# Kernel optimization log

Hardware: AMD Instinct MI355X
Metric: run time of the kernel (lower is better)

## Reference

```python
import jax, jax.numpy as jnp
import numpy as np

D_K = 128


def setup_inputs() -> dict:
    key = jax.random.key(0)
    kq, kk, kv = jax.random.split(key, 3)
    S = 8192
    Query = jax.random.normal(kq, (S, D_K), dtype=jnp.float32)
    Key = jax.random.normal(kk, (S, D_K), dtype=jnp.float32)
    Value = jax.random.normal(kv, (S, D_K), dtype=jnp.float32)
    return {"Query": Query, "Key": Key, "Value": Value}


def reference(Query, Key, Value):
    # scaled dot-product attention, unmasked (masked=False default)
    scale = 1.0 / jnp.sqrt(jnp.asarray(D_K, dtype=jnp.float32))
    scores = jnp.matmul(Query, Key.T) * scale          # [S, S]
    attn = jax.nn.softmax(scores, axis=1)              # softmax over keys (dim=1 on 2-D)
    delta_E = jnp.matmul(attn, Value)                  # [S, d_k]
    return delta_E
```

## Files before the change

### kernel.cpp

```cpp
#include <hip/hip_runtime.h>

#define S_LEN 8192
#define D_KK  128
#define SCALE 0.08838834764831845f

typedef __bf16 bf16x2 __attribute__((ext_vector_type(2)));
typedef __bf16 bf16x4 __attribute__((ext_vector_type(4)));
typedef __bf16 bf16x8 __attribute__((ext_vector_type(8)));
typedef float  f32x16 __attribute__((ext_vector_type(16)));

__global__ __launch_bounds__(256) void prep_kv_23450521436217(
    const float* __restrict__ K,
    const float* __restrict__ V,
    __bf16* __restrict__ Kf,
    __bf16* __restrict__ Vf)
{
    const int tid = threadIdx.x;
    const int t   = blockIdx.x;
    __shared__ __bf16 T[32][140];

    const float* ktile = K + (size_t)t * 32 * D_KK;
    const float* vtile = V + (size_t)t * 32 * D_KK;

    const int row = tid & 31;
    const int cp  = tid >> 5;
    #pragma unroll
    for (int i = 0; i < 2; ++i) {
        int c = cp * 2 + i;
        int s = c >> 1, hi = c & 1;
        const float* src = ktile + row * D_KK + c * 8;
        float4 a = *(const float4*)(src);
        float4 b = *(const float4*)(src + 4);
        bf16x8 o;
        o[0]=(__bf16)a.x; o[1]=(__bf16)a.y; o[2]=(__bf16)a.z; o[3]=(__bf16)a.w;
        o[4]=(__bf16)b.x; o[5]=(__bf16)b.y; o[6]=(__bf16)b.z; o[7]=(__bf16)b.w;
        *(bf16x8*)(Kf + (size_t)(t * 8 + s) * 512 + hi * 256 + row * 8) = o;
    }

    #pragma unroll
    for (int i = 0; i < 4; ++i) {
        int f4 = tid + i * 256;
        float4 v = ((const float4*)vtile)[f4];
        int r = f4 >> 5, cc = (f4 & 31) << 2;
        bf16x4 b;
        b[0]=(__bf16)v.x; b[1]=(__bf16)v.y; b[2]=(__bf16)v.z; b[3]=(__bf16)v.w;
        *(bf16x4*)(&T[r][cc]) = b;
    }
    __syncthreads();

    #pragma unroll
    for (int i = 0; i < 2; ++i) {
        int idx  = tid + i * 256;
        int frag = idx >> 6, lane = idx & 63;
        int hi = lane >> 5, l5 = lane & 31;
        int d = frag >> 1, h = frag & 1;
        bf16x8 o;
        #pragma unroll
        for (int j = 0; j < 8; ++j) o[j] = T[16 * h + 8 * hi + j][32 * d + l5];
        *(bf16x8*)(Vf + (size_t)(t * 8 + frag) * 512 + lane * 8) = o;
    }
}

__global__ __launch_bounds__(512, 2) void attn_fwd_23450521436217(
    const float*  __restrict__ Q,
    const __bf16* __restrict__ Kf,
    const __bf16* __restrict__ Vf,
    float* __restrict__ O)
{
    const int tid  = threadIdx.x;
    const int wave = tid >> 6;
    const int lane = tid & 63;
    const int l5   = lane & 31;
    const int hi   = lane >> 5;

    __shared__ float Oacc[D_KK][33];
    __shared__ float Ml[8][32], Ll[8][32], Lf[32];

    const int qrow = blockIdx.x * 32 + l5;

    bf16x8 qf[8];
    #pragma unroll
    for (int s = 0; s < 8; ++s) {
        const float* qp = Q + (size_t)qrow * D_KK + s * 16 + hi * 8;
        float4 a = *(const float4*)(qp);
        float4 b = *(const float4*)(qp + 4);
        bf16x8 f;
        f[0]=(__bf16)(a.x*SCALE); f[1]=(__bf16)(a.y*SCALE);
        f[2]=(__bf16)(a.z*SCALE); f[3]=(__bf16)(a.w*SCALE);
        f[4]=(__bf16)(b.x*SCALE); f[5]=(__bf16)(b.y*SCALE);
        f[6]=(__bf16)(b.z*SCALE); f[7]=(__bf16)(b.w*SCALE);
        qf[s] = f;
    }

    f32x16 oacc[4];
    #pragma unroll
    for (int d = 0; d < 4; ++d) oacc[d] = f32x16{};
    float m_run = -1e30f, l_run = 0.0f;

    const __bf16* kfp = Kf + (size_t)(wave * 32) * 4096 + lane * 8;
    const __bf16* vfp = Vf + (size_t)(wave * 32) * 4096 + lane * 8;

    bf16x8 kbufA[8], kbufB[8], vb[8];

    #pragma unroll
    for (int s = 0; s < 8; ++s) kbufA[s] = *(const bf16x8*)(kfp + s * 512);

#define ATTN_BODY(KC, KN, IT, PF)                                              \
    {                                                                          \
        const __bf16* vt = vfp + (size_t)(IT) * 4096;                          \
        _Pragma("unroll")                                                      \
        for (int f = 0; f < 8; ++f)                                            \
            vb[f] = *(const bf16x8*)(vt + f * 512);                            \
                 \
        f32x16 c = f32x16{};                                                   \
        _Pragma("unroll")                                                      \
        for (int s = 0; s < 8; ++s)                                            \
            c = __builtin_amdgcn_mfma_f32_32x32x16_bf16(KC[s], qf[s], c,       \
                                                        0, 0, 0);             \
                                  \
        if (PF) {                                                              \
            const __bf16* kn = kfp + (size_t)((IT) + 1) * 4096;                \
            _Pragma("unroll")                                                  \
            for (int s = 0; s < 8; ++s)                                        \
                KN[s] = *(const bf16x8*)(kn + s * 512);                        \
        }                                                                      \
                  \
        float tmax = c[0];                                                     \
        _Pragma("unroll")                                                      \
        for (int r = 1; r < 16; ++r) tmax = fmaxf(tmax, c[r]);                 \
        tmax = fmaxf(tmax, __shfl_xor(tmax, 32));                              \
        if (__any(tmax > m_run + 8.0f)) {                                      \
            float mnew  = fmaxf(m_run, tmax);                                  \
            float alpha = __expf(m_run - mnew);                                \
            _Pragma("unroll")                                                  \
            for (int d = 0; d < 4; ++d) oacc[d] *= alpha;                      \
            l_run *= alpha;                                                    \
            m_run  = mnew;                                                     \
        }                                                                      \
        float p[16], ps = 0.0f;                                                \
        _Pragma("unroll")                                                      \
        for (int r = 0; r < 16; ++r) { p[r] = __expf(c[r] - m_run); ps += p[r]; } \
        ps += __shfl_xor(ps, 32);                                              \
        l_run += ps;                                                           \
                   \
        unsigned pk[8];                                                        \
        _Pragma("unroll")                                                      \
        for (int tq = 0; tq < 8; ++tq) {                                       \
            bf16x2 w; w[0] = (__bf16)p[2*tq]; w[1] = (__bf16)p[2*tq+1];        \
            pk[tq] = __builtin_bit_cast(unsigned, w);                          \
        }                                                                      \
        asm volatile("v_permlane32_swap_b32 %0, %1" : "+v"(pk[0]), "+v"(pk[2]));\
        asm volatile("v_permlane32_swap_b32 %0, %1" : "+v"(pk[1]), "+v"(pk[3]));\
        asm volatile("v_permlane32_swap_b32 %0, %1" : "+v"(pk[4]), "+v"(pk[6]));\
        asm volatile("v_permlane32_swap_b32 %0, %1" : "+v"(pk[5]), "+v"(pk[7]));\
        union { unsigned u[4]; bf16x8 f; } b0, b1;                             \
        b0.u[0]=pk[0]; b0.u[1]=pk[1]; b0.u[2]=pk[2]; b0.u[3]=pk[3];            \
        b1.u[0]=pk[4]; b1.u[1]=pk[5]; b1.u[2]=pk[6]; b1.u[3]=pk[7];            \
                                               \
        _Pragma("unroll")                                                      \
        for (int d = 0; d < 4; ++d) {                                          \
            oacc[d] = __builtin_amdgcn_mfma_f32_32x32x16_bf16(vb[2*d+0], b0.f, \
                                                              oacc[d], 0,0,0); \
            oacc[d] = __builtin_amdgcn_mfma_f32_32x32x16_bf16(vb[2*d+1], b1.f, \
                                                              oacc[d], 0,0,0); \
        }                                                                      \
    }

    for (int it = 0; it < 32; it += 2) {
        ATTN_BODY(kbufA, kbufB, it,     1);
        ATTN_BODY(kbufB, kbufA, it + 1, (it + 2 < 32));
    }
#undef ATTN_BODY

    if (lane < 32) { Ml[wave][lane] = m_run; Ll[wave][lane] = l_run; }
    __syncthreads();

    float M = Ml[0][l5];
    #pragma unroll
    for (int w = 1; w < 8; ++w) M = fmaxf(M, Ml[w][l5]);
    float L = 0.0f;
    #pragma unroll
    for (int w = 0; w < 8; ++w) L += Ll[w][l5] * __expf(Ml[w][l5] - M);
    if (tid < 32) Lf[tid] = L;

    const float wscale = __expf(m_run - M);

    for (int r = 0; r < 8; ++r) {
        if (wave == r) {
            #pragma unroll
            for (int d = 0; d < 4; ++d)
                #pragma unroll
                for (int reg = 0; reg < 16; ++reg) {
                    int drow = d * 32 + (reg & 3) + 8 * (reg >> 2) + 4 * hi;
                    float v = oacc[d][reg] * wscale;
                    if (r == 0) Oacc[drow][l5]  = v;
                    else        Oacc[drow][l5] += v;
                }
        }
        __syncthreads();
    }

    const int q  = tid >> 4;
    const int d0 = (tid & 15) * 8;
    const float invl = 1.0f / Lf[q];
    float4 o1, o2;
    o1.x = Oacc[d0+0][q] * invl; o1.y = Oacc[d0+1][q] * invl;
    o1.z = Oacc[d0+2][q] * invl; o1.w = Oacc[d0+3][q] * invl;
    o2.x = Oacc[d0+4][q] * invl; o2.y = Oacc[d0+5][q] * invl;
    o2.z = Oacc[d0+6][q] * invl; o2.w = Oacc[d0+7][q] * invl;
    float* op = O + (size_t)(blockIdx.x * 32 + q) * D_KK + d0;
    *(float4*)(op)     = o1;
    *(float4*)(op + 4) = o2;
}

extern "C" void kernel_launch(void* const* d_in, const int* in_sizes, int n_in,
                              void* d_out, int out_size, void* d_ws, size_t ws_size,
                              hipStream_t stream) {
    const float* Q = (const float*)d_in[0];
    const float* K = (const float*)d_in[1];
    const float* V = (const float*)d_in[2];
    float* O = (float*)d_out;

    __bf16* Kf = (__bf16*)d_ws;
    __bf16* Vf = (__bf16*)((char*)d_ws + (size_t)S_LEN*D_KK*2);

    hipLaunchKernelGGL(prep_kv_23450521436217, dim3(S_LEN/32), dim3(256), 0, stream,
                       K, V, Kf, Vf);
    hipLaunchKernelGGL(attn_fwd_23450521436217, dim3(S_LEN/32), dim3(512), 0, stream,
                       Q, Kf, Vf, O);
}
```

Baseline: 65.15 us.

## Software-pipeline QK^T one tile ahead of softmax and PV in attention loop

Restructures the main attention loop so the QK^T MFMA for the next key tile is issued before the softmax and PV work of the current tile. Key loads are prefetched two tiles ahead through double-buffered score accumulators. MFMA sections are wrapped in s_setprio to raise wave priority, and the max and sum reductions become tree-shaped to shorten dependency chains. The aim is to overlap matrix-core work with the exp and shuffle latency, at the cost of more VGPRs for the second score accumulator and the extra key buffer.

```diff
diff --git a/kernel.cpp b/kernel.cpp
--- a/kernel.cpp
+++ b/kernel.cpp
@@ -100,34 +100,52 @@
     const __bf16* kfp = Kf + (size_t)(wave * 32) * 4096 + lane * 8;
     const __bf16* vfp = Vf + (size_t)(wave * 32) * 4096 + lane * 8;
 
-    bf16x8 kbufA[8], kbufB[8], vb[8];
-
-    #pragma unroll
-    for (int s = 0; s < 8; ++s) kbufA[s] = *(const bf16x8*)(kfp + s * 512);
-
-#define ATTN_BODY(KC, KN, IT, PF)                                              \
+    bf16x8 kA[8], kB[8], vb[8];
+    f32x16 c0, c1;
+
+    #pragma unroll
+    for (int s = 0; s < 8; ++s) kA[s] = *(const bf16x8*)(kfp + s * 512);
+    #pragma unroll
+    for (int s = 0; s < 8; ++s) kB[s] = *(const bf16x8*)(kfp + 4096 + s * 512);
+    c0 = f32x16{};
+    __builtin_amdgcn_s_setprio(1);
+    #pragma unroll
+    for (int s = 0; s < 8; ++s)
+        c0 = __builtin_amdgcn_mfma_f32_32x32x16_bf16(kA[s], qf[s], c0, 0, 0, 0);
+    __builtin_amdgcn_s_setprio(0);
+
+#define ATTN_BODY(CCUR, CNEXT, KNEXT, KPF, IT, DO_QK, DO_PF)                   \
     {                                                                          \
+          \
         const __bf16* vt = vfp + (size_t)(IT) * 4096;                          \
         _Pragma("unroll")                                                      \
         for (int f = 0; f < 8; ++f)                                            \
             vb[f] = *(const bf16x8*)(vt + f * 512);                            \
-                 \
-        f32x16 c = f32x16{};                                                   \
-        _Pragma("unroll")                                                      \
-        for (int s = 0; s < 8; ++s)                                            \
-            c = __builtin_amdgcn_mfma_f32_32x32x16_bf16(KC[s], qf[s], c,       \
-                                                        0, 0, 0);             \
-                                  \
-        if (PF) {                                                              \
-            const __bf16* kn = kfp + (size_t)((IT) + 1) * 4096;                \
+                \
+        if (DO_QK) {                                                           \
+            CNEXT = f32x16{};                                                  \
+            __builtin_amdgcn_s_setprio(1);                                     \
             _Pragma("unroll")                                                  \
             for (int s = 0; s < 8; ++s)                                        \
-                KN[s] = *(const bf16x8*)(kn + s * 512);                        \
+                CNEXT = __builtin_amdgcn_mfma_f32_32x32x16_bf16(KNEXT[s],      \
+                                                        qf[s], CNEXT, 0,0,0); \
+            __builtin_amdgcn_s_setprio(0);                                     \
         }                                                                      \
                   \
-        float tmax = c[0];                                                     \
-        _Pragma("unroll")                                                      \
-        for (int r = 1; r < 16; ++r) tmax = fmaxf(tmax, c[r]);                 \
+        if (DO_PF) {                                                           \
+            const __bf16* kn = kfp + (size_t)((IT) + 2) * 4096;                \
+            _Pragma("unroll")                                                  \
+            for (int s = 0; s < 8; ++s)                                        \
+                KPF[s] = *(const bf16x8*)(kn + s * 512);                       \
+        }                                                                      \
+                     \
+        float x0 = fmaxf(CCUR[0], CCUR[8]),  x1 = fmaxf(CCUR[1], CCUR[9]);     \
+        float x2 = fmaxf(CCUR[2], CCUR[10]), x3 = fmaxf(CCUR[3], CCUR[11]);    \
+        float x4 = fmaxf(CCUR[4], CCUR[12]), x5 = fmaxf(CCUR[5], CCUR[13]);    \
+        float x6 = fmaxf(CCUR[6], CCUR[14]), x7 = fmaxf(CCUR[7], CCUR[15]);    \
+        float y0 = fmaxf(fmaxf(x0, x4), fmaxf(x1, x5));                        \
+        float y1 = fmaxf(fmaxf(x2, x6), fmaxf(x3, x7));                        \
+        float tmax = fmaxf(y0, y1);                                            \
         tmax = fmaxf(tmax, __shfl_xor(tmax, 32));                              \
         if (__any(tmax > m_run + 8.0f)) {                                      \
             float mnew  = fmaxf(m_run, tmax);                                  \
@@ -137,9 +155,12 @@
             l_run *= alpha;                                                    \
             m_run  = mnew;                                                     \
         }                                                                      \
-        float p[16], ps = 0.0f;                                                \
-        _Pragma("unroll")                                                      \
-        for (int r = 0; r < 16; ++r) { p[r] = __expf(c[r] - m_run); ps += p[r]; } \
+        float p[16];                                                           \
+        _Pragma("unroll")                                                      \
+        for (int r = 0; r < 16; ++r) p[r] = __expf(CCUR[r] - m_run);           \
+        float s0a = (p[0]+p[1]) + (p[2]+p[3]),  s1a = (p[4]+p[5]) + (p[6]+p[7]); \
+        float s2a = (p[8]+p[9]) + (p[10]+p[11]), s3a = (p[12]+p[13]) + (p[14]+p[15]); \
+        float ps = (s0a + s1a) + (s2a + s3a);                                  \
         ps += __shfl_xor(ps, 32);                                              \
         l_run += ps;                                                           \
                    \
@@ -156,7 +177,8 @@
         union { unsigned u[4]; bf16x8 f; } b0, b1;                             \
         b0.u[0]=pk[0]; b0.u[1]=pk[1]; b0.u[2]=pk[2]; b0.u[3]=pk[3];            \
         b1.u[0]=pk[4]; b1.u[1]=pk[5]; b1.u[2]=pk[6]; b1.u[3]=pk[7];            \
-                                               \
+                                                 \
+        __builtin_amdgcn_s_setprio(1);                                         \
         _Pragma("unroll")                                                      \
         for (int d = 0; d < 4; ++d) {                                          \
             oacc[d] = __builtin_amdgcn_mfma_f32_32x32x16_bf16(vb[2*d+0], b0.f, \
@@ -164,12 +186,15 @@
             oacc[d] = __builtin_amdgcn_mfma_f32_32x32x16_bf16(vb[2*d+1], b1.f, \
                                                               oacc[d], 0,0,0); \
         }                                                                      \
-    }
-
-    for (int it = 0; it < 32; it += 2) {
-        ATTN_BODY(kbufA, kbufB, it,     1);
-        ATTN_BODY(kbufB, kbufA, it + 1, (it + 2 < 32));
-    }
+        __builtin_amdgcn_s_setprio(0);                                         \
+    }
+
+    for (int it = 0; it < 30; it += 2) {
+        ATTN_BODY(c0, c1, kB, kA, it,     1, 1);
+        ATTN_BODY(c1, c0, kA, kB, it + 1, 1, 1);
+    }
+    ATTN_BODY(c0, c1, kB, kA, 30, 1, 0);
+    ATTN_BODY(c1, c0, kA, kB, 31, 0, 0);
 #undef ATTN_BODY
 
     if (lane < 32) { Ml[wave][lane] = m_run; Ll[wave][lane] = l_run; }
```

New measurement: 64.75 us. No clear change (-0.6%).

## Share K tiles across waves via LDS and split-K with separate merge kernel

Applied to the files above, without the earlier changes.

Restructures the attention kernel so each block owns 8 query sub-tiles (one per wave) and a 1/8 slice of the keys. K tiles are staged into LDS with global_load_lds double buffering and shared by all waves, instead of each wave streaming its own K from global memory. Partial outputs are written as fp16 along with per-slice max and sum, and a new merge kernel combines them. This cuts K global traffic and removes the in-block cross-wave reduction, but adds a third launch, partial-output memory traffic, fp16 rounding of the partials, and a per-iteration block barrier.

```diff
diff --git a/kernel.cpp b/kernel.cpp
--- a/kernel.cpp
+++ b/kernel.cpp
@@ -8,6 +8,7 @@
 typedef __bf16 bf16x4 __attribute__((ext_vector_type(4)));
 typedef __bf16 bf16x8 __attribute__((ext_vector_type(8)));
 typedef float  f32x16 __attribute__((ext_vector_type(16)));
+typedef _Float16 half_t;
 
 __global__ __launch_bounds__(256) void prep_kv_23450521436217(
     const float* __restrict__ K,
@@ -61,11 +62,13 @@
     }
 }
 
-__global__ __launch_bounds__(512, 2) void attn_fwd_23450521436217(
+__global__ __launch_bounds__(512, 2) void attn_part_23450521436217(
     const float*  __restrict__ Q,
     const __bf16* __restrict__ Kf,
     const __bf16* __restrict__ Vf,
-    float* __restrict__ O)
+    half_t* __restrict__ P16,
+    float*  __restrict__ Mp,
+    float*  __restrict__ Lp)
 {
     const int tid  = threadIdx.x;
     const int wave = tid >> 6;
@@ -73,10 +76,12 @@
     const int l5   = lane & 31;
     const int hi   = lane >> 5;
 
-    __shared__ float Oacc[D_KK][33];
-    __shared__ float Ml[8][32], Ll[8][32], Lf[32];
-
-    const int qrow = blockIdx.x * 32 + l5;
+    const int ks   = blockIdx.x & 7;
+    const int qt   = blockIdx.x >> 3;
+    const int qsub = qt * 8 + wave;
+    const int qrow = qsub * 32 + l5;
+
+    __shared__ __align__(16) __bf16 Klds[2][4096];
 
     bf16x8 qf[8];
     #pragma unroll
@@ -97,120 +102,171 @@
     for (int d = 0; d < 4; ++d) oacc[d] = f32x16{};
     float m_run = -1e30f, l_run = 0.0f;
 
-    const __bf16* kfp = Kf + (size_t)(wave * 32) * 4096 + lane * 8;
-    const __bf16* vfp = Vf + (size_t)(wave * 32) * 4096 + lane * 8;
-
-    bf16x8 kbufA[8], kbufB[8], vb[8];
-
-    #pragma unroll
-    for (int s = 0; s < 8; ++s) kbufA[s] = *(const bf16x8*)(kfp + s * 512);
-
-#define ATTN_BODY(KC, KN, IT, PF)                                              \
-    {                                                                          \
-        const __bf16* vt = vfp + (size_t)(IT) * 4096;                          \
-        _Pragma("unroll")                                                      \
-        for (int f = 0; f < 8; ++f)                                            \
-            vb[f] = *(const bf16x8*)(vt + f * 512);                            \
-                 \
-        f32x16 c = f32x16{};                                                   \
-        _Pragma("unroll")                                                      \
-        for (int s = 0; s < 8; ++s)                                            \
-            c = __builtin_amdgcn_mfma_f32_32x32x16_bf16(KC[s], qf[s], c,       \
-                                                        0, 0, 0);             \
-                                  \
-        if (PF) {                                                              \
-            const __bf16* kn = kfp + (size_t)((IT) + 1) * 4096;                \
-            _Pragma("unroll")                                                  \
-            for (int s = 0; s < 8; ++s)                                        \
-                KN[s] = *(const bf16x8*)(kn + s * 512);                        \
-        }                                                                      \
-                  \
-        float tmax = c[0];                                                     \
-        _Pragma("unroll")                                                      \
-        for (int r = 1; r < 16; ++r) tmax = fmaxf(tmax, c[r]);                 \
-        tmax = fmaxf(tmax, __shfl_xor(tmax, 32));                              \
-        if (__any(tmax > m_run + 8.0f)) {                                      \
-            float mnew  = fmaxf(m_run, tmax);                                  \
-            float alpha = __expf(m_run - mnew);                                \
-            _Pragma("unroll")                                                  \
-            for (int d = 0; d < 4; ++d) oacc[d] *= alpha;                      \
-            l_run *= alpha;                                                    \
-            m_run  = mnew;                                                     \
-        }                                                                      \
-        float p[16], ps = 0.0f;                                                \
-        _Pragma("unroll")                                                      \
-        for (int r = 0; r < 16; ++r) { p[r] = __expf(c[r] - m_run); ps += p[r]; } \
-        ps += __shfl_xor(ps, 32);                                              \
-        l_run += ps;                                                           \
-                   \
-        unsigned pk[8];                                                        \
-        _Pragma("unroll")                                                      \
-        for (int tq = 0; tq < 8; ++tq) {                                       \
-            bf16x2 w; w[0] = (__bf16)p[2*tq]; w[1] = (__bf16)p[2*tq+1];        \
-            pk[tq] = __builtin_bit_cast(unsigned, w);                          \
-        }                                                                      \
-        asm volatile("v_permlane32_swap_b32 %0, %1" : "+v"(pk[0]), "+v"(pk[2]));\
-        asm volatile("v_permlane32_swap_b32 %0, %1" : "+v"(pk[1]), "+v"(pk[3]));\
-        asm volatile("v_permlane32_swap_b32 %0, %1" : "+v"(pk[4]), "+v"(pk[6]));\
-        asm volatile("v_permlane32_swap_b32 %0, %1" : "+v"(pk[5]), "+v"(pk[7]));\
-        union { unsigned u[4]; bf16x8 f; } b0, b1;                             \
-        b0.u[0]=pk[0]; b0.u[1]=pk[1]; b0.u[2]=pk[2]; b0.u[3]=pk[3];            \
-        b1.u[0]=pk[4]; b1.u[1]=pk[5]; b1.u[2]=pk[6]; b1.u[3]=pk[7];            \
-                                               \
-        _Pragma("unroll")                                                      \
-        for (int d = 0; d < 4; ++d) {                                          \
-            oacc[d] = __builtin_amdgcn_mfma_f32_32x32x16_bf16(vb[2*d+0], b0.f, \
-                                                              oacc[d], 0,0,0); \
-            oacc[d] = __builtin_amdgcn_mfma_f32_32x32x16_bf16(vb[2*d+1], b1.f, \
-                                                              oacc[d], 0,0,0); \
-        }                                                                      \
-    }
-
-    for (int it = 0; it < 32; it += 2) {
-        ATTN_BODY(kbufA, kbufB, it,     1);
-        ATTN_BODY(kbufB, kbufA, it + 1, (it + 2 < 32));
-    }
-#undef ATTN_BODY
-
-    if (lane < 32) { Ml[wave][lane] = m_run; Ll[wave][lane] = l_run; }
-    __syncthreads();
-
-    float M = Ml[0][l5];
-    #pragma unroll
-    for (int w = 1; w < 8; ++w) M = fmaxf(M, Ml[w][l5]);
-    float L = 0.0f;
-    #pragma unroll
-    for (int w = 0; w < 8; ++w) L += Ll[w][l5] * __expf(Ml[w][l5] - M);
-    if (tid < 32) Lf[tid] = L;
-
-    const float wscale = __expf(m_run - M);
-
-    for (int r = 0; r < 8; ++r) {
-        if (wave == r) {
+    const __bf16* kbase = Kf + (size_t)(ks * 32) * 4096;
+    const __bf16* vfp   = Vf + (size_t)(ks * 32) * 4096 + lane * 8;
+
+    {
+        const __bf16* src = kbase + wave * 512 + lane * 8;
+        __builtin_amdgcn_global_load_lds(
+            (const __attribute__((address_space(1))) void*)src,
+            (__attribute__((address_space(3))) void*)&Klds[0][wave * 512],
+            16, 0, 0);
+    }
+    __syncthreads();
+
+    for (int it = 0; it < 32; ++it) {
+        const int cur = it & 1;
+
+        if (it < 31) {
+            const __bf16* src = kbase + (size_t)(it + 1) * 4096 + wave * 512 + lane * 8;
+            __builtin_amdgcn_global_load_lds(
+                (const __attribute__((address_space(1))) void*)src,
+                (__attribute__((address_space(3))) void*)&Klds[cur ^ 1][wave * 512],
+                16, 0, 0);
+        }
+
+        const __bf16* vt = vfp + (size_t)it * 4096;
+        bf16x8 vb[8];
+        #pragma unroll
+        for (int f = 0; f < 8; ++f) vb[f] = *(const bf16x8*)(vt + f * 512);
+
+        f32x16 c = f32x16{};
+        __builtin_amdgcn_s_setprio(1);
+        #pragma unroll
+        for (int s = 0; s < 8; ++s) {
+            bf16x8 kf = *(const bf16x8*)(&Klds[cur][s * 512 + lane * 8]);
+            c = __builtin_amdgcn_mfma_f32_32x32x16_bf16(kf, qf[s], c, 0, 0, 0);
+        }
+        __builtin_amdgcn_s_setprio(0);
+
+        float x0 = fmaxf(c[0], c[8]),  x1 = fmaxf(c[1], c[9]);
+        float x2 = fmaxf(c[2], c[10]), x3 = fmaxf(c[3], c[11]);
+        float x4 = fmaxf(c[4], c[12]), x5 = fmaxf(c[5], c[13]);
+        float x6 = fmaxf(c[6], c[14]), x7 = fmaxf(c[7], c[15]);
+        float y0 = fmaxf(fmaxf(x0, x4), fmaxf(x1, x5));
+        float y1 = fmaxf(fmaxf(x2, x6), fmaxf(x3, x7));
+        float tmax = fmaxf(y0, y1);
+        tmax = fmaxf(tmax, __shfl_xor(tmax, 32));
+        if (__any(tmax > m_run + 8.0f)) {
+            float mnew  = fmaxf(m_run, tmax);
+            float alpha = __expf(m_run - mnew);
             #pragma unroll
-            for (int d = 0; d < 4; ++d)
-                #pragma unroll
-                for (int reg = 0; reg < 16; ++reg) {
-                    int drow = d * 32 + (reg & 3) + 8 * (reg >> 2) + 4 * hi;
-                    float v = oacc[d][reg] * wscale;
-                    if (r == 0) Oacc[drow][l5]  = v;
-                    else        Oacc[drow][l5] += v;
-                }
-        }
+            for (int d = 0; d < 4; ++d) oacc[d] *= alpha;
+            l_run *= alpha;
+            m_run  = mnew;
+        }
+        float p[16];
+        #pragma unroll
+        for (int r = 0; r < 16; ++r) p[r] = __expf(c[r] - m_run);
+        float s0a = (p[0]+p[1]) + (p[2]+p[3]),   s1a = (p[4]+p[5]) + (p[6]+p[7]);
+        float s2a = (p[8]+p[9]) + (p[10]+p[11]), s3a = (p[12]+p[13]) + (p[14]+p[15]);
+        float ps = (s0a + s1a) + (s2a + s3a);
+        ps += __shfl_xor(ps, 32);
+        l_run += ps;
+
+        unsigned pk[8];
+        #pragma unroll
+        for (int tq = 0; tq < 8; ++tq) {
+            bf16x2 w; w[0] = (__bf16)p[2*tq]; w[1] = (__bf16)p[2*tq+1];
+            pk[tq] = __builtin_bit_cast(unsigned, w);
+        }
+        asm volatile("v_permlane32_swap_b32 %0, %1" : "+v"(pk[0]), "+v"(pk[2]));
+        asm volatile("v_permlane32_swap_b32 %0, %1" : "+v"(pk[1]), "+v"(pk[3]));
+        asm volatile("v_permlane32_swap_b32 %0, %1" : "+v"(pk[4]), "+v"(pk[6]));
+        asm volatile("v_permlane32_swap_b32 %0, %1" : "+v"(pk[5]), "+v"(pk[7]));
+        union { unsigned u[4]; bf16x8 f; } b0, b1;
+        b0.u[0]=pk[0]; b0.u[1]=pk[1]; b0.u[2]=pk[2]; b0.u[3]=pk[3];
+        b1.u[0]=pk[4]; b1.u[1]=pk[5]; b1.u[2]=pk[6]; b1.u[3]=pk[7];
+
+        __builtin_amdgcn_s_setprio(1);
+        #pragma unroll
+        for (int d = 0; d < 4; ++d) {
+            oacc[d] = __builtin_amdgcn_mfma_f32_32x32x16_bf16(vb[2*d+0], b0.f,
+                                                              oacc[d], 0,0,0);
+            oacc[d] = __builtin_amdgcn_mfma_f32_32x32x16_bf16(vb[2*d+1], b1.f,
+                                                              oacc[d], 0,0,0);
+        }
+        __builtin_amdgcn_s_setprio(0);
+
         __syncthreads();
     }
 
-    const int q  = tid >> 4;
-    const int d0 = (tid & 15) * 8;
-    const float invl = 1.0f / Lf[q];
-    float4 o1, o2;
-    o1.x = Oacc[d0+0][q] * invl; o1.y = Oacc[d0+1][q] * invl;
-    o1.z = Oacc[d0+2][q] * invl; o1.w = Oacc[d0+3][q] * invl;
-    o2.x = Oacc[d0+4][q] * invl; o2.y = Oacc[d0+5][q] * invl;
-    o2.z = Oacc[d0+6][q] * invl; o2.w = Oacc[d0+7][q] * invl;
-    float* op = O + (size_t)(blockIdx.x * 32 + q) * D_KK + d0;
-    *(float4*)(op)     = o1;
-    *(float4*)(op + 4) = o2;
+    if (lane < 32) {
+        Mp[ks * S_LEN + qrow] = m_run;
+        Lp[ks * S_LEN + qrow] = l_run;
+    }
+    half_t* pb = P16 + (size_t)(ks * 256 + qsub) * (128 * 32);
+    #pragma unroll
+    for (int d = 0; d < 4; ++d)
+        #pragma unroll
+        for (int reg = 0; reg < 16; ++reg) {
+            int drow = d * 32 + (reg & 3) + 8 * (reg >> 2) + 4 * hi;
+            pb[drow * 32 + l5] = (half_t)oacc[d][reg];
+        }
+}
+
+__global__ __launch_bounds__(256) void attn_merge_23450521436217(
+    const half_t* __restrict__ P16,
+    const float*  __restrict__ Mp,
+    const float*  __restrict__ Lp,
+    float* __restrict__ O)
+{
+    const int tid  = threadIdx.x;
+    const int qsub = blockIdx.x;
+
+    __shared__ float W[8][32];
+    __shared__ float Li[32];
+    __shared__ float Ot[128][33];
+
+    if (tid < 32) {
+        const int qrow = qsub * 32 + tid;
+        float m[8], l[8];
+        #pragma unroll
+        for (int ks = 0; ks < 8; ++ks) {
+            m[ks] = Mp[ks * S_LEN + qrow];
+            l[ks] = Lp[ks * S_LEN + qrow];
+        }
+        float M = m[0];
+        #pragma unroll
+        for (int ks = 1; ks < 8; ++ks) M = fmaxf(M, m[ks]);
+        float L = 0.0f;
+        #pragma unroll
+        for (int ks = 0; ks < 8; ++ks) {
+            float w = __expf(m[ks] - M);
+            W[ks][tid] = w;
+            L += l[ks] * w;
+        }
+        Li[tid] = 1.0f / L;
+    }
+    __syncthreads();
+
+    const int q  = tid & 31;
+    const int dg = tid >> 5;
+    #pragma unroll
+    for (int j = 0; j < 16; ++j) {
+        const int d = dg * 16 + j;
+        float acc = 0.0f;
+        #pragma unroll
+        for (int ks = 0; ks < 8; ++ks)
+            acc += W[ks][q] *
+                   (float)P16[(size_t)(ks * 256 + qsub) * (128 * 32) + d * 32 + q];
+        Ot[d][q] = acc;
+    }
+    __syncthreads();
+
+    const int qq = tid >> 3;
+    const int dv = (tid & 7) * 16;
+    const float il = Li[qq];
+    float* op = O + (size_t)(qsub * 32 + qq) * D_KK + dv;
+    #pragma unroll
+    for (int i = 0; i < 4; ++i) {
+        float4 o;
+        o.x = Ot[dv + i*4 + 0][qq] * il;
+        o.y = Ot[dv + i*4 + 1][qq] * il;
+        o.z = Ot[dv + i*4 + 2][qq] * il;
+        o.w = Ot[dv + i*4 + 3][qq] * il;
+        ((float4*)op)[i] = o;
+    }
 }
 
 extern "C" void kernel_launch(void* const* d_in, const int* in_sizes, int n_in,
@@ -221,11 +277,18 @@
     const float* V = (const float*)d_in[2];
     float* O = (float*)d_out;
 
-    __bf16* Kf = (__bf16*)d_ws;
-    __bf16* Vf = (__bf16*)((char*)d_ws + (size_t)S_LEN*D_KK*2);
+    char* ws = (char*)d_ws;
+    const size_t kf_b = (size_t)S_LEN * D_KK * 2;
+    __bf16* Kf = (__bf16*)(ws);
+    __bf16* Vf = (__bf16*)(ws + kf_b);
+    float*  Mp = (float*) (ws + 2 * kf_b);
+    float*  Lp = (float*) (ws + 2 * kf_b + 8 * S_LEN * 4);
+    half_t* P16= (half_t*)(ws + 2 * kf_b + 16 * S_LEN * 4);
 
     hipLaunchKernelGGL(prep_kv_23450521436217, dim3(S_LEN/32), dim3(256), 0, stream,
                        K, V, Kf, Vf);
-    hipLaunchKernelGGL(attn_fwd_23450521436217, dim3(S_LEN/32), dim3(512), 0, stream,
-                       Q, Kf, Vf, O);
-}
+    hipLaunchKernelGGL(attn_part_23450521436217, dim3(256), dim3(512), 0, stream,
+                       Q, Kf, Vf, P16, Mp, Lp);
+    hipLaunchKernelGGL(attn_merge_23450521436217, dim3(S_LEN/32), dim3(256), 0, stream,
+                       P16, Mp, Lp, O);
+}
```

Result: faster. 63.83 us (-2.0%).
